# Optimization experiments

Hardware: AMD Instinct MI355X
Metric: run time of the kernel (lower is better)

The kernel has to match this reference:

```python
import jax, jax.numpy as jnp
import numpy as np

H = 128          # num_hidden
NUM_IN = 256     # 2*H: h_E (H) + gathered neighbor h_V (H)
SCALE = 30.0
LN_EPS = 1e-5


def _ln(x, g, b):
    mu = jnp.mean(x, axis=-1, keepdims=True)
    var = jnp.mean((x - mu) ** 2, axis=-1, keepdims=True)
    return (x - mu) * jax.lax.rsqrt(var + LN_EPS) * g + b


def _gather_nodes(nodes, idx):
    # nodes: [B,L,C], idx: [B,L,K] -> [B,L,K,C]
    B = nodes.shape[0]
    return nodes[jnp.arange(B)[:, None, None], idx]


def _mlp3(x, W1, b1, W2, b2, W3, b3):
    h = jax.nn.gelu(x @ W1 + b1, approximate=False)
    h = jax.nn.gelu(h @ W2 + b2, approximate=False)
    return h @ W3 + b3


def setup_inputs() -> dict:
    key = jax.random.key(0)
    ks = jax.random.split(key, 16)
    B, L, K = 2, 2048, 48
    s = 0.02
    inp = {
        "h_V": jax.random.normal(ks[0], (B, L, H), jnp.float32),
        "h_E": jax.random.normal(ks[1], (B, L, K, H), jnp.float32),
        "E_idx": jax.random.randint(ks[2], (B, L, K), 0, L, jnp.int32),
        "mask_V": jnp.ones((B, L), jnp.float32),
        "mask_attend": jnp.ones((B, L, K), jnp.float32),
        # node-update MLP
        "W1": jax.random.normal(ks[3], (H + NUM_IN, H), jnp.float32) * s,
        "b1": jnp.zeros((H,), jnp.float32),
        "W2": jax.random.normal(ks[4], (H, H), jnp.float32) * s,
        "b2": jnp.zeros((H,), jnp.float32),
        "W3": jax.random.normal(ks[5], (H, H), jnp.float32) * s,
        "b3": jnp.zeros((H,), jnp.float32),
        # edge-update MLP
        "W11": jax.random.normal(ks[6], (H + NUM_IN, H), jnp.float32) * s,
        "b11": jnp.zeros((H,), jnp.float32),
        "W12": jax.random.normal(ks[7], (H, H), jnp.float32) * s,
        "b12": jnp.zeros((H,), jnp.float32),
        "W13": jax.random.normal(ks[8], (H, H), jnp.float32) * s,
        "b13": jnp.zeros((H,), jnp.float32),
        # position-wise FFN (H -> 4H -> H)
        "Win": jax.random.normal(ks[9], (H, 4 * H), jnp.float32) * s,
        "bin": jnp.zeros((4 * H,), jnp.float32),
        "Wout": jax.random.normal(ks[10], (4 * H, H), jnp.float32) * s,
        "bout": jnp.zeros((H,), jnp.float32),
        # LayerNorms
        "g1": jnp.ones((H,), jnp.float32), "be1": jnp.zeros((H,), jnp.float32),
        "g2": jnp.ones((H,), jnp.float32), "be2": jnp.zeros((H,), jnp.float32),
        "g3": jnp.ones((H,), jnp.float32), "be3": jnp.zeros((H,), jnp.float32),
    }
    return inp


def reference(h_V, h_E, E_idx, mask_V, mask_attend,
              W1, b1, W2, b2, W3, b3,
              W11, b11, W12, b12, W13, b13,
              Win, bin, Wout, bout,
              g1, be1, g2, be2, g3, be3):
    K = h_E.shape[-2]
    # --- node update: gather, concat, 3-layer MLP, masked mean-sum, LN residual ---
    h_nbr = _gather_nodes(h_V, E_idx)                               # [B,L,K,H]
    h_V_exp = jnp.broadcast_to(h_V[:, :, None, :], h_nbr.shape)     # [B,L,K,H]
    h_EV = jnp.concatenate([h_V_exp, h_E, h_nbr], axis=-1)          # [B,L,K,3H]
    h_msg = _mlp3(h_EV, W1, b1, W2, b2, W3, b3)                     # [B,L,K,H]
    h_msg = mask_attend[..., None] * h_msg
    dh = jnp.sum(h_msg, axis=-2) / SCALE                            # [B,L,H]
    h_V = _ln(h_V + dh, g1, be1)
    # position-wise FFN + LN residual
    dh = jax.nn.gelu(h_V @ Win + bin, approximate=False) @ Wout + bout
    h_V = _ln(h_V + dh, g2, be2)
    h_V = mask_V[..., None] * h_V
    # --- edge update ---
    h_nbr = _gather_nodes(h_V, E_idx)
    h_V_exp = jnp.broadcast_to(h_V[:, :, None, :], h_nbr.shape)
    h_EV = jnp.concatenate([h_V_exp, h_E, h_nbr], axis=-1)
    h_msg = _mlp3(h_EV, W11, b11, W12, b12, W13, b13)
    h_E = _ln(h_E + h_msg, g3, be3)
    return (h_V, h_E)
```

## Files before the change

### kernel.cpp

```cpp
#include <hip/hip_runtime.h>
#include <hip/hip_bf16.h>

typedef __attribute__((ext_vector_type(8))) short short8;
typedef __attribute__((ext_vector_type(4))) float f32x4;

__device__ inline short f2bf(float f) {
    unsigned u = __builtin_bit_cast(unsigned, f);
    u += 0x7fffu + ((u >> 16) & 1u);
    return (short)(u >> 16);
}
__device__ inline float bf2f(short s) {
    return __builtin_bit_cast(float, ((unsigned)(unsigned short)s) << 16);
}
__device__ inline float gelu_fast(float x) {
    float z = x * (1.0f + 0.044715f * x * x);
    float e = __expf(1.5957691216f * z);
    return x - x * __builtin_amdgcn_rcpf(e + 1.0f);
}
__device__ inline float wred(float s) {
#pragma unroll
    for (int o = 32; o; o >>= 1) s += __shfl_xor(s, o, 64);
    return s;
}

__global__ void pack_all_kernel(const float* __restrict__ W1, const float* __restrict__ W2,
                                const float* __restrict__ W3, const float* __restrict__ W11,
                                const float* __restrict__ W12, const float* __restrict__ W13,
                                const float* __restrict__ Win, const float* __restrict__ Wout,
                                short* __restrict__ out) {
    int b = blockIdx.x;
    if (b < 80) {
        int which = b >> 3;
        const float* Ws[10] = {W1 + 128 * 128, W2, W3, W11 + 128 * 128, W12, W13,
                               W1, W1 + 256 * 128, W11, W11 + 256 * 128};
        const float* W = Ws[which];
        int i = (b & 7) * 256 + threadIdx.x;
        int lane = i & 63, tile = i >> 6;
        int kt = tile & 3, nt = tile >> 2;
        int n = nt * 16 + (lane & 15);
        int k0 = kt * 32 + (lane >> 4) * 8;
        short8 v;
#pragma unroll
        for (int j = 0; j < 8; ++j) v[j] = f2bf(W[(size_t)(k0 + j) * 128 + n]);
        *(short8*)(out + (size_t)which * 16384 + (size_t)i * 8) = v;
    } else if (b < 112) {
        int i = (b - 80) * 256 + threadIdx.x;
        int lane = i & 63, tile = i >> 6;
        int kt = tile & 3, nt = tile >> 2;
        int n = nt * 16 + (lane & 15);
        int k0 = kt * 32 + (lane >> 4) * 8;
        short8 v;
#pragma unroll
        for (int j = 0; j < 8; ++j) v[j] = f2bf(Win[(size_t)(k0 + j) * 512 + n]);
        *(short8*)(out + 163840 + (size_t)i * 8) = v;
    } else {
        int i = (b - 112) * 256 + threadIdx.x;
        int lane = i & 63, tile = i >> 6;
        int kt = tile & 15, nt = tile >> 4;
        int n = nt * 16 + (lane & 15);
        int k0 = kt * 32 + (lane >> 4) * 8;
        short8 v;
#pragma unroll
        for (int j = 0; j < 8; ++j) v[j] = f2bf(Wout[(size_t)(k0 + j) * 128 + n]);
        *(short8*)(out + 229376 + (size_t)i * 8) = v;
    }
}

__global__ __launch_bounds__(256) void node_pre_kernel(
    const float* __restrict__ hV, const short8* __restrict__ Bs,
    const short8* __restrict__ Bn, const float* __restrict__ bias,
    float* __restrict__ Ys, short* __restrict__ Yn) {
    int n0 = blockIdx.x * 16;
    int tid = threadIdx.x, lane = tid & 63, w = tid >> 6;
    __shared__ __align__(16) short A_sw[16 * 128];
    {
        int off = tid * 8;
        int r = off >> 7, c0 = off & 127;
        const float* src = hV + (size_t)n0 * 128 + off;
        float4 f0 = *(const float4*)(src);
        float4 f1 = *(const float4*)(src + 4);
        short8 v;
        v[0] = f2bf(f0.x); v[1] = f2bf(f0.y); v[2] = f2bf(f0.z); v[3] = f2bf(f0.w);
        v[4] = f2bf(f1.x); v[5] = f2bf(f1.y); v[6] = f2bf(f1.z); v[7] = f2bf(f1.w);
        *(short8*)((char*)A_sw + r * 256 + ((c0 * 2) ^ ((r & 7) << 4))) = v;
    }
    __syncthreads();
    const short8* Bp = (w < 2) ? Bs : Bn;
    f32x4 acc[4];
#pragma unroll
    for (int n2 = 0; n2 < 4; ++n2) acc[n2] = (f32x4){0.f, 0.f, 0.f, 0.f};
#pragma unroll
    for (int kt = 0; kt < 4; ++kt) {
        int row = lane & 15;
        int kb = (kt * 32 + (lane >> 4) * 8) * 2;
        short8 a = *(const short8*)((const char*)A_sw + row * 256 + (kb ^ ((row & 7) << 4)));
#pragma unroll
        for (int n2 = 0; n2 < 4; ++n2) {
            int ntl = (w & 1) * 4 + n2;
            short8 bf = Bp[(ntl * 4 + kt) * 64 + lane];
            acc[n2] = __builtin_amdgcn_mfma_f32_16x16x32_bf16(a, bf, acc[n2], 0, 0, 0);
        }
    }
    if (w < 2) {
#pragma unroll
        for (int n2 = 0; n2 < 4; ++n2) {
            int col = ((w & 1) * 4 + n2) * 16 + (lane & 15);
            float bv = bias[col];
#pragma unroll
            for (int i = 0; i < 4; ++i) {
                int row = (lane >> 4) * 4 + i;
                Ys[(size_t)(n0 + row) * 128 + col] = acc[n2][i] + bv;
            }
        }
    } else {
#pragma unroll
        for (int n2 = 0; n2 < 4; ++n2) {
            int col = ((w & 1) * 4 + n2) * 16 + (lane & 15);
#pragma unroll
            for (int i = 0; i < 4; ++i) {
                int row = (lane >> 4) * 4 + i;
                Yn[(size_t)(n0 + row) * 128 + col] = f2bf(acc[n2][i]);
            }
        }
    }
}

__device__ inline void gemm48(const short* A_sw, const short8* __restrict__ Bp,
                              int w, int lane, f32x4 acc[3][2]) {
#pragma unroll
    for (int mt = 0; mt < 3; ++mt)
#pragma unroll
        for (int n2 = 0; n2 < 2; ++n2) acc[mt][n2] = (f32x4){0.f, 0.f, 0.f, 0.f};
#pragma unroll
    for (int kt = 0; kt < 4; ++kt) {
        short8 a[3];
        int kb = (kt * 32 + (lane >> 4) * 8) * 2;
#pragma unroll
        for (int mt = 0; mt < 3; ++mt) {
            int row = mt * 16 + (lane & 15);
            a[mt] = *(const short8*)((const char*)A_sw + row * 256 + (kb ^ ((row & 7) << 4)));
        }
#pragma unroll
        for (int n2 = 0; n2 < 2; ++n2) {
            short8 bf = Bp[((w * 2 + n2) * 4 + kt) * 64 + lane];
#pragma unroll
            for (int mt = 0; mt < 3; ++mt)
                acc[mt][n2] = __builtin_amdgcn_mfma_f32_16x16x32_bf16(a[mt], bf, acc[mt][n2], 0, 0, 0);
        }
    }
}

__device__ inline void stage_hE(const float* __restrict__ Eb, short* A_sw, int tid,
                                short* Eres ) {
#pragma unroll
    for (int i = 0; i < 3; ++i) {
        int e = tid + i * 256;
        int r = e >> 4, c0 = (e & 15) * 8;
        float4 f0 = *(const float4*)(Eb + r * 128 + c0);
        float4 f1 = *(const float4*)(Eb + r * 128 + c0 + 4);
        short8 v;
        v[0] = f2bf(f0.x); v[1] = f2bf(f0.y); v[2] = f2bf(f0.z); v[3] = f2bf(f0.w);
        v[4] = f2bf(f1.x); v[5] = f2bf(f1.y); v[6] = f2bf(f1.z); v[7] = f2bf(f1.w);
        *(short8*)((char*)A_sw + r * 256 + ((c0 * 2) ^ ((r & 7) << 4))) = v;
        if (Eres) *(short8*)(Eres + r * 136 + c0) = v;
    }
}

__device__ inline void gather_Yn(const short* __restrict__ Yng, const int* __restrict__ Eidx,
                                 int node, int bb, int tid, short* Ygb) {
    if (tid < 192) {
        int r = tid >> 2, q = tid & 3;
        int idx = Eidx[node * 48 + r];
        const short8* src = (const short8*)(Yng + ((size_t)bb * 2048 + idx) * 128 + q * 32);
        short8* dst = (short8*)(Ygb + r * 136 + q * 32);
        dst[0] = src[0];
        dst[1] = src[1];
        dst[2] = src[2];
        dst[3] = src[3];
    }
}

__global__ __launch_bounds__(256) void node_msg_kernel(
    const float* __restrict__ hV, const float* __restrict__ hE,
    const int* __restrict__ Eidx, const float* __restrict__ maskAtt,
    const short8* __restrict__ W1bp, const short8* __restrict__ W2p,
    const short8* __restrict__ W3p, const float* __restrict__ b2,
    const float* __restrict__ b3, const float* __restrict__ Ysg,
    const short* __restrict__ Yng, const float* __restrict__ g1,
    const float* __restrict__ be1, float* __restrict__ hv1out) {
    const int node = blockIdx.x;
    const int bb = node >> 11;
    const int tid = threadIdx.x;
    const int lane = tid & 63, w = tid >> 6;

    __shared__ __align__(16) short A_sw[48 * 128];
    __shared__ __align__(16) short Ygb[48 * 136];
    __shared__ float Ysh[128];
    __shared__ float mask_s[48];
    __shared__ float red[8];

    stage_hE(hE + (size_t)node * 6144, A_sw, tid, nullptr);
    if (tid < 128) Ysh[tid] = Ysg[(size_t)node * 128 + tid];
    if (tid >= 128 && tid < 176) mask_s[tid - 128] = maskAtt[node * 48 + tid - 128];
    gather_Yn(Yng, Eidx, node, bb, tid, Ygb);
    __syncthreads();

    f32x4 acc[3][2];
    gemm48(A_sw, W1bp, w, lane, acc);
    __syncthreads();
#pragma unroll
    for (int mt = 0; mt < 3; ++mt)
#pragma unroll
        for (int n2 = 0; n2 < 2; ++n2) {
            int col = (w * 2 + n2) * 16 + (lane & 15);
            float ysv = Ysh[col];
#pragma unroll
            for (int i = 0; i < 4; ++i) {
                int row = mt * 16 + (lane >> 4) * 4 + i;
                float v = acc[mt][n2][i] + ysv + bf2f(Ygb[row * 136 + col]);
                v = gelu_fast(v);
                *(short*)((char*)A_sw + row * 256 + ((col * 2) ^ ((row & 7) << 4))) = f2bf(v);
            }
        }
    __syncthreads();
    gemm48(A_sw, W2p, w, lane, acc);
    __syncthreads();
#pragma unroll
    for (int mt = 0; mt < 3; ++mt)
#pragma unroll
        for (int n2 = 0; n2 < 2; ++n2) {
            int col = (w * 2 + n2) * 16 + (lane & 15);
            float bv = b2[col];
#pragma unroll
            for (int i = 0; i < 4; ++i) {
                int row = mt * 16 + (lane >> 4) * 4 + i;
                float v = gelu_fast(acc[mt][n2][i] + bv);
                *(short*)((char*)A_sw + row * 256 + ((col * 2) ^ ((row & 7) << 4))) = f2bf(v);
            }
        }
    __syncthreads();
    gemm48(A_sw, W3p, w, lane, acc);
    float u[2];
#pragma unroll
    for (int n2 = 0; n2 < 2; ++n2) {
        int col = (w * 2 + n2) * 16 + (lane & 15);
        float b3c = b3[col];
        float s = 0.f;
#pragma unroll
        for (int mt = 0; mt < 3; ++mt)
#pragma unroll
            for (int i = 0; i < 4; ++i) {
                int row = mt * 16 + (lane >> 4) * 4 + i;
                s += (acc[mt][n2][i] + b3c) * mask_s[row];
            }
        s += __shfl_xor(s, 16, 64);
        s += __shfl_xor(s, 32, 64);
        u[n2] = hV[(size_t)node * 128 + col] + s * (1.0f / 30.0f);
    }
    float ps = wred(u[0] + u[1]) * 0.25f;
    float pq = wred(u[0] * u[0] + u[1] * u[1]) * 0.25f;
    if (lane == 0) { red[w] = ps; red[4 + w] = pq; }
    __syncthreads();
    float S = red[0] + red[1] + red[2] + red[3];
    float Q = red[4] + red[5] + red[6] + red[7];
    float mu = S * (1.0f / 128.0f);
    float var = Q * (1.0f / 128.0f) - mu * mu;
    float rs = rsqrtf(var + 1e-5f);
    if ((lane >> 4) == 0) {
#pragma unroll
        for (int n2 = 0; n2 < 2; ++n2) {
            int col = (w * 2 + n2) * 16 + (lane & 15);
            hv1out[(size_t)node * 128 + col] = (u[n2] - mu) * rs * g1[col] + be1[col];
        }
    }
}

__global__ __launch_bounds__(256) void ffn_kernel(
    const float* __restrict__ hv1, const short8* __restrict__ Winp,
    const float* __restrict__ binp, const short8* __restrict__ Woutp,
    const float* __restrict__ bout, const float* __restrict__ g2,
    const float* __restrict__ be2, const float* __restrict__ maskV,
    float* __restrict__ hVout) {
    int n0 = blockIdx.x * 16;
    int tid = threadIdx.x, lane = tid & 63, w = tid >> 6;
    __shared__ float X[16 * 128];
    __shared__ __align__(16) short A_sw[16 * 128];
    __shared__ __align__(16) short H_sw[16 * 512];

    {
        int off = tid * 8;
        int r = off >> 7, c0 = off & 127;
        const float* src = hv1 + (size_t)n0 * 128 + off;
        float4 f0 = *(const float4*)(src);
        float4 f1 = *(const float4*)(src + 4);
        *(float4*)(&X[off]) = f0;
        *(float4*)(&X[off + 4]) = f1;
        short8 v;
        v[0] = f2bf(f0.x); v[1] = f2bf(f0.y); v[2] = f2bf(f0.z); v[3] = f2bf(f0.w);
        v[4] = f2bf(f1.x); v[5] = f2bf(f1.y); v[6] = f2bf(f1.z); v[7] = f2bf(f1.w);
        *(short8*)((char*)A_sw + r * 256 + ((c0 * 2) ^ ((r & 7) << 4))) = v;
    }
    __syncthreads();

    f32x4 acc1[8];
#pragma unroll
    for (int n2 = 0; n2 < 8; ++n2) acc1[n2] = (f32x4){0.f, 0.f, 0.f, 0.f};
#pragma unroll
    for (int kt = 0; kt < 4; ++kt) {
        int row = lane & 15;
        int kb = (kt * 32 + (lane >> 4) * 8) * 2;
        short8 a = *(const short8*)((const char*)A_sw + row * 256 + (kb ^ ((row & 7) << 4)));
#pragma unroll
        for (int n2 = 0; n2 < 8; ++n2) {
            short8 bf = Winp[((w * 8 + n2) * 4 + kt) * 64 + lane];
            acc1[n2] = __builtin_amdgcn_mfma_f32_16x16x32_bf16(a, bf, acc1[n2], 0, 0, 0);
        }
    }
#pragma unroll
    for (int n2 = 0; n2 < 8; ++n2) {
        int col = (w * 8 + n2) * 16 + (lane & 15);
        float bv = binp[col];
#pragma unroll
        for (int i = 0; i < 4; ++i) {
            int row = (lane >> 4) * 4 + i;
            float v = gelu_fast(acc1[n2][i] + bv);
            *(short*)((char*)H_sw + row * 1024 + ((col * 2) ^ ((row & 7) << 4))) = f2bf(v);
        }
    }
    __syncthreads();

    f32x4 acc2[2];
    acc2[0] = (f32x4){0.f, 0.f, 0.f, 0.f};
    acc2[1] = (f32x4){0.f, 0.f, 0.f, 0.f};
#pragma unroll
    for (int kt = 0; kt < 16; ++kt) {
        int row = lane & 15;
        int kb = (kt * 32 + (lane >> 4) * 8) * 2;
        short8 a = *(const short8*)((const char*)H_sw + row * 1024 + (kb ^ ((row & 7) << 4)));
#pragma unroll
        for (int n2 = 0; n2 < 2; ++n2) {
            short8 bf = Woutp[((w * 2 + n2) * 16 + kt) * 64 + lane];
            acc2[n2] = __builtin_amdgcn_mfma_f32_16x16x32_bf16(a, bf, acc2[n2], 0, 0, 0);
        }
    }
#pragma unroll
    for (int n2 = 0; n2 < 2; ++n2) {
        int col = (w * 2 + n2) * 16 + (lane & 15);
        float bo = bout[col];
#pragma unroll
        for (int i = 0; i < 4; ++i) {
            int row = (lane >> 4) * 4 + i;
            X[row * 128 + col] += acc2[n2][i] + bo;
        }
    }
    __syncthreads();

#pragma unroll
    for (int p = 0; p < 4; ++p) {
        int r = p * 4 + w;
        float u0 = X[r * 128 + lane], u1 = X[r * 128 + lane + 64];
        float s = wred(u0 + u1);
        float q = wred(u0 * u0 + u1 * u1);
        float mu = s * (1.0f / 128.0f);
        float var = q * (1.0f / 128.0f) - mu * mu;
        float rs = rsqrtf(var + 1e-5f);
        float mv = maskV[n0 + r];
        hVout[(size_t)(n0 + r) * 128 + lane] = mv * ((u0 - mu) * rs * g2[lane] + be2[lane]);
        hVout[(size_t)(n0 + r) * 128 + lane + 64] = mv * ((u1 - mu) * rs * g2[lane + 64] + be2[lane + 64]);
    }
}

__global__ __launch_bounds__(256) void edge_upd_kernel(
    const float* __restrict__ hE, const int* __restrict__ Eidx,
    const short8* __restrict__ W11bp, const short8* __restrict__ W12p,
    const short8* __restrict__ W13p, const float* __restrict__ b12,
    const float* __restrict__ b13, const float* __restrict__ Ysg,
    const short* __restrict__ Yng, const float* __restrict__ g3,
    const float* __restrict__ be3, float* __restrict__ hEout) {
    const int node = blockIdx.x;
    const int bb = node >> 11;
    const int tid = threadIdx.x;
    const int lane = tid & 63, w = tid >> 6;

    __shared__ __align__(16) short A_sw[48 * 128];
    __shared__ __align__(16) short Ygb[48 * 136];
    __shared__ __align__(16) short Eres[48 * 136];
    __shared__ float Ysh[128];

    stage_hE(hE + (size_t)node * 6144, A_sw, tid, Eres);
    if (tid < 128) Ysh[tid] = Ysg[(size_t)node * 128 + tid];
    gather_Yn(Yng, Eidx, node, bb, tid, Ygb);
    __syncthreads();

    f32x4 acc[3][2];
    gemm48(A_sw, W11bp, w, lane, acc);
    __syncthreads();
#pragma unroll
    for (int mt = 0; mt < 3; ++mt)
#pragma unroll
        for (int n2 = 0; n2 < 2; ++n2) {
            int col = (w * 2 + n2) * 16 + (lane & 15);
            float ysv = Ysh[col];
#pragma unroll
            for (int i = 0; i < 4; ++i) {
                int row = mt * 16 + (lane >> 4) * 4 + i;
                float v = acc[mt][n2][i] + ysv + bf2f(Ygb[row * 136 + col]);
                v = gelu_fast(v);
                *(short*)((char*)A_sw + row * 256 + ((col * 2) ^ ((row & 7) << 4))) = f2bf(v);
            }
        }
    __syncthreads();
    gemm48(A_sw, W12p, w, lane, acc);
    __syncthreads();
#pragma unroll
    for (int mt = 0; mt < 3; ++mt)
#pragma unroll
        for (int n2 = 0; n2 < 2; ++n2) {
            int col = (w * 2 + n2) * 16 + (lane & 15);
            float bv = b12[col];
#pragma unroll
            for (int i = 0; i < 4; ++i) {
                int row = mt * 16 + (lane >> 4) * 4 + i;
                float v = gelu_fast(acc[mt][n2][i] + bv);
                *(short*)((char*)A_sw + row * 256 + ((col * 2) ^ ((row & 7) << 4))) = f2bf(v);
            }
        }
    __syncthreads();
    gemm48(A_sw, W13p, w, lane, acc);
#pragma unroll
    for (int mt = 0; mt < 3; ++mt)
#pragma unroll
        for (int n2 = 0; n2 < 2; ++n2) {
            int col = (w * 2 + n2) * 16 + (lane & 15);
            float bv = b13[col];
#pragma unroll
            for (int i = 0; i < 4; ++i) {
                int row = mt * 16 + (lane >> 4) * 4 + i;
                float v = acc[mt][n2][i] + bv + bf2f(Eres[row * 136 + col]);
                Ygb[row * 136 + col] = f2bf(v);
            }
        }
    __syncthreads();

    float* outb = hEout + (size_t)node * 6144;
    float gl0 = g3[lane], gl1 = g3[lane + 64];
    float bl0 = be3[lane], bl1 = be3[lane + 64];
#pragma unroll
    for (int p = 0; p < 12; ++p) {
        int r = p * 4 + w;
        float u0 = bf2f(Ygb[r * 136 + lane]);
        float u1 = bf2f(Ygb[r * 136 + lane + 64]);
        float s = wred(u0 + u1);
        float q = wred(u0 * u0 + u1 * u1);
        float mu = s * (1.0f / 128.0f);
        float var = q * (1.0f / 128.0f) - mu * mu;
        float rs = rsqrtf(var + 1e-5f);
        outb[r * 128 + lane] = (u0 - mu) * rs * gl0 + bl0;
        outb[r * 128 + lane + 64] = (u1 - mu) * rs * gl1 + bl1;
    }
}

extern "C" void kernel_launch(void* const* d_in, const int* in_sizes, int n_in,
                              void* d_out, int out_size, void* d_ws, size_t ws_size,
                              hipStream_t stream) {
    const float* hV      = (const float*)d_in[0];
    const float* hE      = (const float*)d_in[1];
    const int*   Eidx    = (const int*)d_in[2];
    const float* maskV   = (const float*)d_in[3];
    const float* maskAtt = (const float*)d_in[4];
    const float* W1  = (const float*)d_in[5];
    const float* b1  = (const float*)d_in[6];
    const float* W2  = (const float*)d_in[7];
    const float* b2  = (const float*)d_in[8];
    const float* W3  = (const float*)d_in[9];
    const float* b3  = (const float*)d_in[10];
    const float* W11 = (const float*)d_in[11];
    const float* b11 = (const float*)d_in[12];
    const float* W12 = (const float*)d_in[13];
    const float* b12 = (const float*)d_in[14];
    const float* W13 = (const float*)d_in[15];
    const float* b13 = (const float*)d_in[16];
    const float* Win = (const float*)d_in[17];
    const float* binp= (const float*)d_in[18];
    const float* Wout= (const float*)d_in[19];
    const float* bout= (const float*)d_in[20];
    const float* g1  = (const float*)d_in[21];
    const float* be1 = (const float*)d_in[22];
    const float* g2  = (const float*)d_in[23];
    const float* be2 = (const float*)d_in[24];
    const float* g3  = (const float*)d_in[25];
    const float* be3 = (const float*)d_in[26];

    char* ws = (char*)d_ws;
    short* Wpk  = (short*)ws;
    float* Ys   = (float*)(ws + 1048576);
    short* Yn   = (short*)(ws + 1048576 + 2097152);
    float* hv1  = (float*)(ws + 1048576 + 2097152 + 1048576);

    float* hVout = (float*)d_out;
    float* hEout = hVout + 2 * 2048 * 128;

    const int NNODE = 2 * 2048;

    pack_all_kernel<<<144, 256, 0, stream>>>(W1, W2, W3, W11, W12, W13, Win, Wout, Wpk);

    node_pre_kernel<<<NNODE / 16, 256, 0, stream>>>(hV,
        (const short8*)(Wpk + 98304), (const short8*)(Wpk + 114688), b1, Ys, Yn);

    node_msg_kernel<<<NNODE, 256, 0, stream>>>(hV, hE, Eidx, maskAtt,
        (const short8*)(Wpk), (const short8*)(Wpk + 16384), (const short8*)(Wpk + 32768),
        b2, b3, Ys, Yn, g1, be1, hv1);

    ffn_kernel<<<NNODE / 16, 256, 0, stream>>>(hv1,
        (const short8*)(Wpk + 163840), binp, (const short8*)(Wpk + 229376), bout,
        g2, be2, maskV, hVout);

    node_pre_kernel<<<NNODE / 16, 256, 0, stream>>>(hVout,
        (const short8*)(Wpk + 131072), (const short8*)(Wpk + 147456), b11, Ys, Yn);

    edge_upd_kernel<<<NNODE, 256, 0, stream>>>(hE, Eidx,
        (const short8*)(Wpk + 49152), (const short8*)(Wpk + 65536), (const short8*)(Wpk + 81920),
        b12, b13, Ys, Yn, g3, be3, hEout);
}
```

Before: 141.7 us.

## Swap MFMA operands for first two MLP layers and pack bf16 epilogue stores

The first two MLP GEMMs in the node-message and edge-update kernels now put weights as the A operand and edges as the B operand. Each lane therefore holds four consecutive features for one edge, so the epilogues can write packed 8-byte bf16 stores into shared memory instead of scalar 2-byte stores. Float-to-bf16 conversion now uses the hardware v_cvt_pk_bf16_f32 instruction, replacing the software rounding. The edge kernel drops the Eres shared buffer and rereads the fp32 residual from global memory, which cuts LDS use and may raise occupancy at the cost of extra global reads (likely cache hits).

Measured after the change: 134.9 us. 4.8% less time.

```diff
diff --git a/kernel.cpp b/kernel.cpp
--- a/kernel.cpp
+++ b/kernel.cpp
@@ -11,6 +11,11 @@
 }
 __device__ inline float bf2f(short s) {
     return __builtin_bit_cast(float, ((unsigned)(unsigned short)s) << 16);
+}
+__device__ inline unsigned cvt_pk_bf16(float a, float b) {
+    unsigned r;
+    asm("v_cvt_pk_bf16_f32 %0, %1, %2" : "=v"(r) : "v"(a), "v"(b));
+    return r;
 }
 __device__ inline float gelu_fast(float x) {
     float z = x * (1.0f + 0.044715f * x * x);
@@ -79,10 +84,10 @@
         const float* src = hV + (size_t)n0 * 128 + off;
         float4 f0 = *(const float4*)(src);
         float4 f1 = *(const float4*)(src + 4);
-        short8 v;
-        v[0] = f2bf(f0.x); v[1] = f2bf(f0.y); v[2] = f2bf(f0.z); v[3] = f2bf(f0.w);
-        v[4] = f2bf(f1.x); v[5] = f2bf(f1.y); v[6] = f2bf(f1.z); v[7] = f2bf(f1.w);
-        *(short8*)((char*)A_sw + r * 256 + ((c0 * 2) ^ ((r & 7) << 4))) = v;
+        uint4 u;
+        u.x = cvt_pk_bf16(f0.x, f0.y); u.y = cvt_pk_bf16(f0.z, f0.w);
+        u.z = cvt_pk_bf16(f1.x, f1.y); u.w = cvt_pk_bf16(f1.z, f1.w);
+        *(uint4*)((char*)A_sw + r * 256 + ((c0 * 2) ^ ((r & 7) << 4))) = u;
     }
     __syncthreads();
     const short8* Bp = (w < 2) ? Bs : Bn;
@@ -125,8 +130,9 @@
     }
 }
 
-__device__ inline void gemm48(const short* A_sw, const short8* __restrict__ Bp,
-                              int w, int lane, f32x4 acc[3][2]) {
+
+__device__ inline void gemm48_a(const short* A_sw, const short8* __restrict__ Wp,
+                                int w, int lane, f32x4 acc[3][2]) {
 #pragma unroll
     for (int mt = 0; mt < 3; ++mt)
 #pragma unroll
@@ -142,7 +148,7 @@
         }
 #pragma unroll
         for (int n2 = 0; n2 < 2; ++n2) {
-            short8 bf = Bp[((w * 2 + n2) * 4 + kt) * 64 + lane];
+            short8 bf = Wp[((w * 2 + n2) * 4 + kt) * 64 + lane];
 #pragma unroll
             for (int mt = 0; mt < 3; ++mt)
                 acc[mt][n2] = __builtin_amdgcn_mfma_f32_16x16x32_bf16(a[mt], bf, acc[mt][n2], 0, 0, 0);
@@ -150,19 +156,42 @@
     }
 }
 
-__device__ inline void stage_hE(const float* __restrict__ Eb, short* A_sw, int tid,
-                                short* Eres ) {
+__device__ inline void gemm48_swz(const short* A_sw, const short8* __restrict__ Wp,
+                                  int w, int lane, f32x4 acc[2][3]) {
+#pragma unroll
+    for (int m2 = 0; m2 < 2; ++m2)
+#pragma unroll
+        for (int nt = 0; nt < 3; ++nt) acc[m2][nt] = (f32x4){0.f, 0.f, 0.f, 0.f};
+#pragma unroll
+    for (int kt = 0; kt < 4; ++kt) {
+        int kb = (kt * 32 + (lane >> 4) * 8) * 2;
+        short8 e[3];
+#pragma unroll
+        for (int nt = 0; nt < 3; ++nt) {
+            int row = nt * 16 + (lane & 15);
+            e[nt] = *(const short8*)((const char*)A_sw + row * 256 + (kb ^ ((row & 7) << 4)));
+        }
+#pragma unroll
+        for (int m2 = 0; m2 < 2; ++m2) {
+            short8 wf = Wp[((w * 2 + m2) * 4 + kt) * 64 + lane];
+#pragma unroll
+            for (int nt = 0; nt < 3; ++nt)
+                acc[m2][nt] = __builtin_amdgcn_mfma_f32_16x16x32_bf16(wf, e[nt], acc[m2][nt], 0, 0, 0);
+        }
+    }
+}
+
+__device__ inline void stage_hE(const float* __restrict__ Eb, short* A_sw, int tid) {
 #pragma unroll
     for (int i = 0; i < 3; ++i) {
         int e = tid + i * 256;
         int r = e >> 4, c0 = (e & 15) * 8;
         float4 f0 = *(const float4*)(Eb + r * 128 + c0);
         float4 f1 = *(const float4*)(Eb + r * 128 + c0 + 4);
-        short8 v;
-        v[0] = f2bf(f0.x); v[1] = f2bf(f0.y); v[2] = f2bf(f0.z); v[3] = f2bf(f0.w);
-        v[4] = f2bf(f1.x); v[5] = f2bf(f1.y); v[6] = f2bf(f1.z); v[7] = f2bf(f1.w);
-        *(short8*)((char*)A_sw + r * 256 + ((c0 * 2) ^ ((r & 7) << 4))) = v;
-        if (Eres) *(short8*)(Eres + r * 136 + c0) = v;
+        uint4 u;
+        u.x = cvt_pk_bf16(f0.x, f0.y); u.y = cvt_pk_bf16(f0.z, f0.w);
+        u.z = cvt_pk_bf16(f1.x, f1.y); u.w = cvt_pk_bf16(f1.z, f1.w);
+        *(uint4*)((char*)A_sw + r * 256 + ((c0 * 2) ^ ((r & 7) << 4))) = u;
     }
 }
 
@@ -177,6 +206,46 @@
         dst[1] = src[1];
         dst[2] = src[2];
         dst[3] = src[3];
+    }
+}
+
+__device__ inline void epi_l1(f32x4 acc[2][3], const float* Ysh, const short* Ygb,
+                              short* A_sw, int w, int lane) {
+#pragma unroll
+    for (int m2 = 0; m2 < 2; ++m2) {
+        int featb = (w * 2 + m2) * 16 + ((lane >> 4) << 2);
+        float ys0 = Ysh[featb], ys1 = Ysh[featb + 1];
+        float ys2 = Ysh[featb + 2], ys3 = Ysh[featb + 3];
+#pragma unroll
+        for (int nt = 0; nt < 3; ++nt) {
+            int edge = nt * 16 + (lane & 15);
+            uint2 yv = *(const uint2*)(Ygb + edge * 136 + featb);
+            float v0 = gelu_fast(acc[m2][nt][0] + ys0 + __builtin_bit_cast(float, yv.x << 16));
+            float v1 = gelu_fast(acc[m2][nt][1] + ys1 + __builtin_bit_cast(float, yv.x & 0xffff0000u));
+            float v2 = gelu_fast(acc[m2][nt][2] + ys2 + __builtin_bit_cast(float, yv.y << 16));
+            float v3 = gelu_fast(acc[m2][nt][3] + ys3 + __builtin_bit_cast(float, yv.y & 0xffff0000u));
+            uint2 pk = {cvt_pk_bf16(v0, v1), cvt_pk_bf16(v2, v3)};
+            *(uint2*)((char*)A_sw + edge * 256 + ((featb * 2) ^ ((edge & 7) << 4))) = pk;
+        }
+    }
+}
+
+__device__ inline void epi_l2(f32x4 acc[2][3], const float* __restrict__ b,
+                              short* A_sw, int w, int lane) {
+#pragma unroll
+    for (int m2 = 0; m2 < 2; ++m2) {
+        int featb = (w * 2 + m2) * 16 + ((lane >> 4) << 2);
+        float b0 = b[featb], b1 = b[featb + 1], b2v = b[featb + 2], b3v = b[featb + 3];
+#pragma unroll
+        for (int nt = 0; nt < 3; ++nt) {
+            int edge = nt * 16 + (lane & 15);
+            float v0 = gelu_fast(acc[m2][nt][0] + b0);
+            float v1 = gelu_fast(acc[m2][nt][1] + b1);
+            float v2 = gelu_fast(acc[m2][nt][2] + b2v);
+            float v3 = gelu_fast(acc[m2][nt][3] + b3v);
+            uint2 pk = {cvt_pk_bf16(v0, v1), cvt_pk_bf16(v2, v3)};
+            *(uint2*)((char*)A_sw + edge * 256 + ((featb * 2) ^ ((edge & 7) << 4))) = pk;
+        }
     }
 }
 
@@ -199,47 +268,24 @@
     __shared__ float mask_s[48];
     __shared__ float red[8];
 
-    stage_hE(hE + (size_t)node * 6144, A_sw, tid, nullptr);
+    stage_hE(hE + (size_t)node * 6144, A_sw, tid);
     if (tid < 128) Ysh[tid] = Ysg[(size_t)node * 128 + tid];
     if (tid >= 128 && tid < 176) mask_s[tid - 128] = maskAtt[node * 48 + tid - 128];
     gather_Yn(Yng, Eidx, node, bb, tid, Ygb);
     __syncthreads();
 
-    f32x4 acc[3][2];
-    gemm48(A_sw, W1bp, w, lane, acc);
-    __syncthreads();
-#pragma unroll
-    for (int mt = 0; mt < 3; ++mt)
-#pragma unroll
-        for (int n2 = 0; n2 < 2; ++n2) {
-            int col = (w * 2 + n2) * 16 + (lane & 15);
-            float ysv = Ysh[col];
-#pragma unroll
-            for (int i = 0; i < 4; ++i) {
-                int row = mt * 16 + (lane >> 4) * 4 + i;
-                float v = acc[mt][n2][i] + ysv + bf2f(Ygb[row * 136 + col]);
-                v = gelu_fast(v);
-                *(short*)((char*)A_sw + row * 256 + ((col * 2) ^ ((row & 7) << 4))) = f2bf(v);
-            }
-        }
-    __syncthreads();
-    gemm48(A_sw, W2p, w, lane, acc);
-    __syncthreads();
-#pragma unroll
-    for (int mt = 0; mt < 3; ++mt)
-#pragma unroll
-        for (int n2 = 0; n2 < 2; ++n2) {
-            int col = (w * 2 + n2) * 16 + (lane & 15);
-            float bv = b2[col];
-#pragma unroll
-            for (int i = 0; i < 4; ++i) {
-                int row = mt * 16 + (lane >> 4) * 4 + i;
-                float v = gelu_fast(acc[mt][n2][i] + bv);
-                *(short*)((char*)A_sw + row * 256 + ((col * 2) ^ ((row & 7) << 4))) = f2bf(v);
-            }
-        }
-    __syncthreads();
-    gemm48(A_sw, W3p, w, lane, acc);
+    f32x4 acc[2][3];
+    gemm48_swz(A_sw, W1bp, w, lane, acc);
+    __syncthreads();
+    epi_l1(acc, Ysh, Ygb, A_sw, w, lane);
+    __syncthreads();
+    gemm48_swz(A_sw, W2p, w, lane, acc);
+    __syncthreads();
+    epi_l2(acc, b2, A_sw, w, lane);
+    __syncthreads();
+
+    f32x4 acc3[3][2];
+    gemm48_a(A_sw, W3p, w, lane, acc3);
     float u[2];
 #pragma unroll
     for (int n2 = 0; n2 < 2; ++n2) {
@@ -251,7 +297,7 @@
 #pragma unroll
             for (int i = 0; i < 4; ++i) {
                 int row = mt * 16 + (lane >> 4) * 4 + i;
-                s += (acc[mt][n2][i] + b3c) * mask_s[row];
+                s += (acc3[mt][n2][i] + b3c) * mask_s[row];
             }
         s += __shfl_xor(s, 16, 64);
         s += __shfl_xor(s, 32, 64);
@@ -295,10 +341,10 @@
         float4 f1 = *(const float4*)(src + 4);
         *(float4*)(&X[off]) = f0;
         *(float4*)(&X[off + 4]) = f1;
-        short8 v;
-        v[0] = f2bf(f0.x); v[1] = f2bf(f0.y); v[2] = f2bf(f0.z); v[3] = f2bf(f0.w);
-        v[4] = f2bf(f1.x); v[5] = f2bf(f1.y); v[6] = f2bf(f1.z); v[7] = f2bf(f1.w);
-        *(short8*)((char*)A_sw + r * 256 + ((c0 * 2) ^ ((r & 7) << 4))) = v;
+        uint4 u;
+        u.x = cvt_pk_bf16(f0.x, f0.y); u.y = cvt_pk_bf16(f0.z, f0.w);
+        u.z = cvt_pk_bf16(f1.x, f1.y); u.w = cvt_pk_bf16(f1.z, f1.w);
+        *(uint4*)((char*)A_sw + r * 256 + ((c0 * 2) ^ ((r & 7) << 4))) = u;
     }
     __syncthreads();
 
@@ -384,49 +430,26 @@
 
     __shared__ __align__(16) short A_sw[48 * 128];
     __shared__ __align__(16) short Ygb[48 * 136];
-    __shared__ __align__(16) short Eres[48 * 136];
     __shared__ float Ysh[128];
 
-    stage_hE(hE + (size_t)node * 6144, A_sw, tid, Eres);
+    const float* Eb = hE + (size_t)node * 6144;
+    stage_hE(Eb, A_sw, tid);
     if (tid < 128) Ysh[tid] = Ysg[(size_t)node * 128 + tid];
     gather_Yn(Yng, Eidx, node, bb, tid, Ygb);
     __syncthreads();
 
-    f32x4 acc[3][2];
-    gemm48(A_sw, W11bp, w, lane, acc);
-    __syncthreads();
-#pragma unroll
-    for (int mt = 0; mt < 3; ++mt)
-#pragma unroll
-        for (int n2 = 0; n2 < 2; ++n2) {
-            int col = (w * 2 + n2) * 16 + (lane & 15);
-            float ysv = Ysh[col];
-#pragma unroll
-            for (int i = 0; i < 4; ++i) {
-                int row = mt * 16 + (lane >> 4) * 4 + i;
-                float v = acc[mt][n2][i] + ysv + bf2f(Ygb[row * 136 + col]);
-                v = gelu_fast(v);
-                *(short*)((char*)A_sw + row * 256 + ((col * 2) ^ ((row & 7) << 4))) = f2bf(v);
-            }
-        }
-    __syncthreads();
-    gemm48(A_sw, W12p, w, lane, acc);
-    __syncthreads();
-#pragma unroll
-    for (int mt = 0; mt < 3; ++mt)
-#pragma unroll
-        for (int n2 = 0; n2 < 2; ++n2) {
-            int col = (w * 2 + n2) * 16 + (lane & 15);
-            float bv = b12[col];
-#pragma unroll
-            for (int i = 0; i < 4; ++i) {
-                int row = mt * 16 + (lane >> 4) * 4 + i;
-                float v = gelu_fast(acc[mt][n2][i] + bv);
-                *(short*)((char*)A_sw + row * 256 + ((col * 2) ^ ((row & 7) << 4))) = f2bf(v);
-            }
-        }
-    __syncthreads();
-    gemm48(A_sw, W13p, w, lane, acc);
+    f32x4 acc[2][3];
+    gemm48_swz(A_sw, W11bp, w, lane, acc);
+    __syncthreads();
+    epi_l1(acc, Ysh, Ygb, A_sw, w, lane);
+    __syncthreads();
+    gemm48_swz(A_sw, W12p, w, lane, acc);
+    __syncthreads();
+    epi_l2(acc, b12, A_sw, w, lane);
+    __syncthreads();
+
+    f32x4 acc3[3][2];
+    gemm48_a(A_sw, W13p, w, lane, acc3);
 #pragma unroll
     for (int mt = 0; mt < 3; ++mt)
 #pragma unroll
@@ -436,7 +459,7 @@
 #pragma unroll
             for (int i = 0; i < 4; ++i) {
                 int row = mt * 16 + (lane >> 4) * 4 + i;
-                float v = acc[mt][n2][i] + bv + bf2f(Eres[row * 136 + col]);
+                float v = acc3[mt][n2][i] + bv + Eb[row * 128 + col];
                 Ygb[row * 136 + col] = f2bf(v);
             }
         }
```
